# Kernel tuning notes

Hardware: AMD Instinct MI355X
Metric: run time of the kernel (lower is better)

Reference implementation:

```python
import jax, jax.numpy as jnp
import numpy as np

D_MODEL = 768
NHEAD = 12
HEAD_DIM = D_MODEL // NHEAD


def setup_inputs() -> dict:
    key = jax.random.key(0)
    ks = jax.random.split(key, 9)
    B, T = 4, 2048
    s = 1.0 / np.sqrt(D_MODEL)
    inp = {
        "x": jax.random.normal(ks[0], (B, T, D_MODEL), dtype=jnp.float32),
        "Wq": jax.random.normal(ks[1], (D_MODEL, D_MODEL), dtype=jnp.float32) * s,
        "bq": jnp.zeros((D_MODEL,), dtype=jnp.float32),
        "Wk": jax.random.normal(ks[2], (D_MODEL, D_MODEL), dtype=jnp.float32) * s,
        "bk": jnp.zeros((D_MODEL,), dtype=jnp.float32),
        "Wv": jax.random.normal(ks[3], (D_MODEL, D_MODEL), dtype=jnp.float32) * s,
        "bv": jnp.zeros((D_MODEL,), dtype=jnp.float32),
        "Wo": jax.random.normal(ks[4], (D_MODEL, D_MODEL), dtype=jnp.float32) * s,
        "bo": jnpp_zeros(ks) if False else jnp.zeros((D_MODEL,), dtype=jnp.float32),
    }
    return inp


def reference(x, Wq, bq, Wk, bk, Wv, bv, Wo, bo):
    B, T, _ = x.shape
    # projections (torch Linear: y = x @ W.T + b; here W stored as [in, out])
    q = (x @ Wq + bq).reshape(B, T, NHEAD, HEAD_DIM).transpose(0, 2, 1, 3)
    k = (x @ Wk + bk).reshape(B, T, NHEAD, HEAD_DIM).transpose(0, 2, 1, 3)
    v = (x @ Wv + bv).reshape(B, T, NHEAD, HEAD_DIM).transpose(0, 2, 1, 3)
    scale = 1.0 / np.sqrt(HEAD_DIM).astype(np.float32)
    scores = jnp.einsum("bhqd,bhkd->bhqk", q, k) * scale  # [B,H,T,T]
    attn = jax.nn.softmax(scores, axis=-1)
    out = jnp.einsum("bhqk,bhkd->bhqd", attn, v)  # [B,H,T,hd]
    out = out.transpose(0, 2, 1, 3).reshape(B, T, D_MODEL)
    return out @ Wo + bo
```

## Files before the change

### kernel.cpp

```cpp
#include <hip/hip_runtime.h>
#include <hip/hip_bf16.h>

#define DM 768
#define HD 64
#define NH 12
#define TT 2048
#define BB 4
#define MM 8192
#define BHH 48

typedef short bfx8 __attribute__((ext_vector_type(8)));
typedef short bfx4 __attribute__((ext_vector_type(4)));
typedef float f32x4 __attribute__((ext_vector_type(4)));
typedef float f32x16 __attribute__((ext_vector_type(16)));
typedef int i32x4 __attribute__((ext_vector_type(4)));
typedef unsigned uix2 __attribute__((ext_vector_type(2)));

__device__ __forceinline__ unsigned short f2bf(float f) {
  unsigned u = __float_as_uint(f);
  u += 0x7fffu + ((u >> 16) & 1u);
  return (unsigned short)(u >> 16);
}

__device__ __forceinline__ unsigned short f2bf_hw(float f) {
  return __builtin_bit_cast(unsigned short, __float2bfloat16(f));
}

__device__ __forceinline__ float fexp2(float x) {
#if __has_builtin(__builtin_amdgcn_exp2f)
  return __builtin_amdgcn_exp2f(x);
#else
  return __expf(x * 0.6931471805599453f);
#endif
}

__device__ __forceinline__ unsigned cvt_pk_bf16(float lo, float hi) {
  unsigned r;
  asm("v_cvt_pk_bf16_f32 %0, %1, %2" : "=v"(r) : "v"(lo), "v"(hi));
  return r;
}

__device__ __forceinline__ void pl32swap(unsigned& a, unsigned& b) {
#if __has_builtin(__builtin_amdgcn_permlane32_swap)
  uix2 r = __builtin_amdgcn_permlane32_swap(a, b, false, false);
  a = r.x; b = r.y;
#else
  asm volatile("v_permlane32_swap_b32 %0, %1" : "+v"(a), "+v"(b));
#endif
}

typedef const __attribute__((address_space(1))) void* gas_p;
typedef __attribute__((address_space(3))) void* las_p;
__device__ __forceinline__ void gld16(const void* g, void* l) {
  __builtin_amdgcn_global_load_lds((gas_p)g, (las_p)l, 16, 0, 0);
}

__global__ __launch_bounds__(256) void xconv(const float* __restrict__ x,
                                             short* __restrict__ xb, int n4) {
  int i = blockIdx.x * blockDim.x + threadIdx.x;
  int stride = gridDim.x * blockDim.x;
  for (; i < n4; i += stride) {
    float4 v = ((const float4*)x)[i];
    short4 o;
    o.x = (short)f2bf(v.x); o.y = (short)f2bf(v.y);
    o.z = (short)f2bf(v.z); o.w = (short)f2bf(v.w);
    ((short4*)xb)[i] = o;
  }
}

__global__ __launch_bounds__(256) void wconv_all(
    const float* __restrict__ W0, const float* __restrict__ W1,
    const float* __restrict__ W2, const float* __restrict__ W3,
    short* __restrict__ WtBase) {
  __shared__ float tile[32][33];
  int z = blockIdx.z;
  const float* W = z == 0 ? W0 : z == 1 ? W1 : z == 2 ? W2 : W3;
  short* Wt = WtBase + (size_t)z * (DM * DM);
  int kb = blockIdx.x * 32, nb = blockIdx.y * 32;
  int tx = threadIdx.x, ty = threadIdx.y;
#pragma unroll
  for (int i = 0; i < 4; ++i)
    tile[ty + 8 * i][tx] = W[(kb + ty + 8 * i) * DM + nb + tx];
  __syncthreads();
#pragma unroll
  for (int i = 0; i < 4; ++i)
    Wt[(nb + ty + 8 * i) * DM + kb + tx] = (short)f2bf(tile[tx][ty + 8 * i]);
}

template <int QKV>
__global__ __launch_bounds__(256) void gemm_k(
    const short* __restrict__ A, const short* __restrict__ Bt0,
    const float* __restrict__ b0, const float* __restrict__ b1,
    const float* __restrict__ b2, void* __restrict__ o0,
    void* __restrict__ o1, void* __restrict__ o2) {
  __shared__ __align__(16) short As[2][128 * 32];
  __shared__ __align__(16) short Bs[2][128 * 32];
  const int tid = threadIdx.x;
  const int lane = tid & 63, w = tid >> 6;
  const int ln15 = lane & 15, lg = lane >> 4;
  const int ny = blockIdx.y;
  const int mat = QKV ? (ny / 6) : 0;
  const int n0 = QKV ? (ny % 6) * 128 : ny * 128;
  const int mode = QKV ? (mat == 2 ? 1 : 0) : 2;
  const short* Bt = Bt0 + (size_t)mat * (DM * DM);
  const float* bias = QKV ? (mat == 0 ? b0 : mat == 1 ? b1 : b2) : b0;
  void* out = QKV ? (mat == 0 ? o0 : mat == 1 ? o1 : o2) : o0;
  const int m0 = blockIdx.x * 128;
  const int wm = w >> 1, wn = w & 1;

  f32x4 acc[4][4];
#pragma unroll
  for (int i = 0; i < 4; ++i)
#pragma unroll
    for (int j = 0; j < 4; ++j) acc[i][j] = f32x4{0.f, 0.f, 0.f, 0.f};

  auto stage = [&](int buf, int k0) {
#pragma unroll
    for (int j = 0; j < 2; ++j) {
      int c = w * 128 + j * 64 + lane;
      int row = c >> 2, cb = c & 3;
      int scb = cb ^ ((row >> 1) & 3);
      gld16(A + (m0 + row) * DM + k0 + (scb << 3), &As[buf][(w * 128 + j * 64) * 8]);
      gld16(Bt + (n0 + row) * DM + k0 + (scb << 3), &Bs[buf][(w * 128 + j * 64) * 8]);
    }
  };

  stage(0, 0);
  __syncthreads();

  for (int t = 0; t < 24; ++t) {
    int buf = t & 1;
    if (t + 1 < 24) stage(buf ^ 1, (t + 1) * 32);
    bfx8 af[4], bfr[4];
#pragma unroll
    for (int mt = 0; mt < 4; ++mt) {
      int row = wm * 64 + mt * 16 + ln15;
      int byt = (lg * 16) ^ (((row >> 1) & 3) << 4);
      af[mt] = *(const bfx8*)(&As[buf][row * 32 + (byt >> 1)]);
    }
#pragma unroll
    for (int nt = 0; nt < 4; ++nt) {
      int row = wn * 64 + nt * 16 + ln15;
      int byt = (lg * 16) ^ (((row >> 1) & 3) << 4);
      bfr[nt] = *(const bfx8*)(&Bs[buf][row * 32 + (byt >> 1)]);
    }
#pragma unroll
    for (int mt = 0; mt < 4; ++mt)
#pragma unroll
      for (int nt = 0; nt < 4; ++nt)
        acc[mt][nt] = __builtin_amdgcn_mfma_f32_16x16x32_bf16(af[mt], bfr[nt], acc[mt][nt], 0, 0, 0);
    __syncthreads();
  }

  float bv[4];
#pragma unroll
  for (int nt = 0; nt < 4; ++nt) bv[nt] = bias[n0 + wn * 64 + nt * 16 + ln15];

#pragma unroll
  for (int mt = 0; mt < 4; ++mt) {
#pragma unroll
    for (int nt = 0; nt < 4; ++nt) {
      int n = n0 + wn * 64 + nt * 16 + ln15;
      int mbase = m0 + wm * 64 + mt * 16 + lg * 4;
      if (mode == 2) {
        float* fo = (float*)out;
#pragma unroll
        for (int r = 0; r < 4; ++r)
          fo[(long)(mbase + r) * DM + n] = acc[mt][nt][r] + bv[nt];
      } else {
        short* so = (short*)out;
        int b = mbase >> 11, tt = mbase & 2047, h = n >> 6, d = n & 63;
        if (mode == 0) {
#pragma unroll
          for (int r = 0; r < 4; ++r)
            so[((long)(b * NH + h) * TT + tt + r) * HD + d] = (short)f2bf(acc[mt][nt][r] + bv[nt]);
        } else {
          bfx4 pk;
#pragma unroll
          for (int r = 0; r < 4; ++r) pk[r] = (short)f2bf(acc[mt][nt][r] + bv[nt]);
          *(bfx4*)(&so[((long)(b * NH + h) * HD + d) * TT + tt]) = pk;
        }
      }
    }
  }
}

__global__ __launch_bounds__(256) void attn_fwd(
    const short* __restrict__ Q, const short* __restrict__ K,
    const short* __restrict__ Vt, short* __restrict__ O) {
  __shared__ __align__(16) short Ks[2][64 * 64];
  __shared__ __align__(16) short Vs[2][64 * 64];
  const int tid = threadIdx.x, lane = tid & 63, w = tid >> 6;
  const int l31 = lane & 31, hi = lane >> 5;
  const int qt = blockIdx.x, bh = blockIdx.y;
  const int q0 = qt * 128 + w * 32;
  const short* Kh = K + (long)bh * TT * HD;
  const short* Vh = Vt + (long)bh * HD * TT;
  const float CEXP = 0.18033688011112042f;
  const float BIAS = 8.0f;

  bfx8 qf[4];
#pragma unroll
  for (int c = 0; c < 4; ++c)
    qf[c] = *(const bfx8*)(Q + ((long)bh * TT + q0 + l31) * HD + c * 16 + hi * 8);

  const int sw = (l31 & 7) << 4;
  const int base0 = l31 * 128, base1 = base0 + 4096;
  int col[4];
#pragma unroll
  for (int c = 0; c < 4; ++c) col[c] = (c * 32 + hi * 16) ^ sw;

  const short* kg[2];
  const short* vg[2];
#pragma unroll
  for (int j = 0; j < 2; ++j) {
    int c = w * 128 + j * 64 + lane;
    int row = c >> 3, cb = c & 7, scb = cb ^ (row & 7);
    kg[j] = Kh + row * HD + scb * 8;
    vg[j] = Vh + (long)row * TT + scb * 8;
  }

  auto stage = [&](int buf) {
#pragma unroll
    for (int j = 0; j < 2; ++j) {
      gld16(kg[j], (char*)Ks + buf * 8192 + (w * 128 + j * 64) * 16);
      gld16(vg[j], (char*)Vs + buf * 8192 + (w * 128 + j * 64) * 16);
    }
    kg[0] += 64 * HD; kg[1] += 64 * HD;
    vg[0] += 64;      vg[1] += 64;
  };

  f32x16 oacc[2];
#pragma unroll
  for (int db = 0; db < 2; ++db)
#pragma unroll
    for (int i = 0; i < 16; ++i) oacc[db][i] = 0.f;
  float lp = 0.f;

  stage(0);
  __syncthreads();

#pragma unroll 1
  for (int tp = 0; tp < 16; ++tp) {
#pragma unroll
    for (int half = 0; half < 2; ++half) {
      const int t = tp * 2 + half;
      if (t + 1 < 32) stage(half ^ 1);
      const char* ksb = (const char*)Ks + half * 8192;
      const char* vsb = (const char*)Vs + half * 8192;

      f32x16 sacc[2];
#pragma unroll
      for (int kvb = 0; kvb < 2; ++kvb) {
        f32x16 s;
#pragma unroll
        for (int i = 0; i < 16; ++i) s[i] = 0.f;
        const int rb = kvb ? base1 : base0;
#pragma unroll
        for (int c = 0; c < 4; ++c) {
          bfx8 kf = *(const bfx8*)(ksb + rb + col[c]);
          s = __builtin_amdgcn_mfma_f32_32x32x16_bf16(kf, qf[c], s, 0, 0, 0);
        }
        sacc[kvb] = s;
      }

      bfx8 pf[4];
#pragma unroll
      for (int kvb = 0; kvb < 2; ++kvb) {
        float pv[16];
#pragma unroll
        for (int r = 0; r < 16; ++r) {
          pv[r] = fexp2(__builtin_fmaf(sacc[kvb][r], CEXP, -BIAS));
          lp += pv[r];
        }
        unsigned g0a = cvt_pk_bf16(pv[0], pv[1]),   g0b = cvt_pk_bf16(pv[2], pv[3]);
        unsigned g1a = cvt_pk_bf16(pv[4], pv[5]),   g1b = cvt_pk_bf16(pv[6], pv[7]);
        unsigned g2a = cvt_pk_bf16(pv[8], pv[9]),   g2b = cvt_pk_bf16(pv[10], pv[11]);
        unsigned g3a = cvt_pk_bf16(pv[12], pv[13]), g3b = cvt_pk_bf16(pv[14], pv[15]);
        pl32swap(g0a, g1a); pl32swap(g0b, g1b);
        pl32swap(g2a, g3a); pl32swap(g2b, g3b);
        i32x4 f0 = {(int)g0a, (int)g0b, (int)g1a, (int)g1b};
        i32x4 f1 = {(int)g2a, (int)g2b, (int)g3a, (int)g3b};
        pf[kvb * 2]     = __builtin_bit_cast(bfx8, f0);
        pf[kvb * 2 + 1] = __builtin_bit_cast(bfx8, f1);
      }

#pragma unroll
      for (int db = 0; db < 2; ++db) {
        const int rb = db ? base1 : base0;
#pragma unroll
        for (int kt = 0; kt < 4; ++kt) {
          bfx8 vf = *(const bfx8*)(vsb + rb + col[kt]);
          oacc[db] = __builtin_amdgcn_mfma_f32_32x32x16_bf16(pf[kt], vf, oacc[db], 0, 0, 0);
        }
      }
      __syncthreads();
    }
  }

  lp += __shfl_xor(lp, 32);
  float linv = 1.f / lp;
  float lv[16];
#pragma unroll
  for (int g = 0; g < 4; ++g)
#pragma unroll
    for (int r = 0; r < 4; ++r) lv[g * 4 + r] = __shfl(linv, 8 * g + 4 * hi + r);
  const int b = bh / NH, h = bh - b * NH;
#pragma unroll
  for (int db = 0; db < 2; ++db)
#pragma unroll
    for (int g = 0; g < 4; ++g)
#pragma unroll
      for (int r = 0; r < 4; ++r) {
        int q = q0 + 8 * g + 4 * hi + r;
        O[(long)(b * TT + q) * DM + h * HD + db * 32 + l31] =
            (short)f2bf_hw(oacc[db][g * 4 + r] * lv[g * 4 + r]);
      }
}

extern "C" void kernel_launch(void* const* d_in, const int* in_sizes, int n_in,
                              void* d_out, int out_size, void* d_ws, size_t ws_size,
                              hipStream_t stream) {
  const float* x  = (const float*)d_in[0];
  const float* Wq = (const float*)d_in[1];
  const float* bq = (const float*)d_in[2];
  const float* Wk = (const float*)d_in[3];
  const float* bk = (const float*)d_in[4];
  const float* Wv = (const float*)d_in[5];
  const float* bv = (const float*)d_in[6];
  const float* Wo = (const float*)d_in[7];
  const float* bo = (const float*)d_in[8];
  float* out = (float*)d_out;

  char* ws = (char*)d_ws;
  short* xb  = (short*)(ws);
  short* WqT = (short*)(ws + 12582912);
  short* WoT = (short*)(ws + 16121856);
  short* Qb  = (short*)(ws + 17301504);
  short* Kb  = (short*)(ws + 29884416);
  short* Vtb = (short*)(ws + 42467328);
  short* Ob  = xb;

  xconv<<<2048, 256, 0, stream>>>(x, xb, MM * DM / 4);
  wconv_all<<<dim3(24, 24, 4), dim3(32, 8), 0, stream>>>(Wq, Wk, Wv, Wo, WqT);
  gemm_k<1><<<dim3(64, 18), 256, 0, stream>>>(xb, WqT, bq, bk, bv, Qb, Kb, Vtb);
  attn_fwd<<<dim3(16, BHH), 256, 0, stream>>>(Qb, Kb, Vtb, Ob);
  gemm_k<0><<<dim3(64, 6), 256, 0, stream>>>(Ob, WoT, bo, bo, bo, out, out, out);
}
```

Measured before the change: 236.5 us.

## Restructure attention to 64 queries per wave, read V from global, fuse prep kernels

The attention kernel now runs two waves per block, and each wave handles 64 queries (two 32-row tiles). Every K fragment loaded from LDS therefore feeds two MFMAs. V is no longer staged in LDS: it is read straight from global memory into registers, which halves LDS use per block. The block index is remapped so blocks that share a head are grouped together for L2 locality. The x and weight conversion kernels are merged into one launch to save a kernel launch. In exchange, register pressure rises and V loads are now exposed to global latency.

```diff
diff --git a/kernel.cpp b/kernel.cpp
--- a/kernel.cpp
+++ b/kernel.cpp
@@ -55,36 +55,41 @@
   __builtin_amdgcn_global_load_lds((gas_p)g, (las_p)l, 16, 0, 0);
 }
 
-__global__ __launch_bounds__(256) void xconv(const float* __restrict__ x,
-                                             short* __restrict__ xb, int n4) {
-  int i = blockIdx.x * blockDim.x + threadIdx.x;
-  int stride = gridDim.x * blockDim.x;
-  for (; i < n4; i += stride) {
-    float4 v = ((const float4*)x)[i];
-    short4 o;
-    o.x = (short)f2bf(v.x); o.y = (short)f2bf(v.y);
-    o.z = (short)f2bf(v.z); o.w = (short)f2bf(v.w);
-    ((short4*)xb)[i] = o;
-  }
-}
-
-__global__ __launch_bounds__(256) void wconv_all(
+__global__ __launch_bounds__(256) void prep(
+    const float* __restrict__ x, short* __restrict__ xb,
     const float* __restrict__ W0, const float* __restrict__ W1,
     const float* __restrict__ W2, const float* __restrict__ W3,
     short* __restrict__ WtBase) {
-  __shared__ float tile[32][33];
-  int z = blockIdx.z;
-  const float* W = z == 0 ? W0 : z == 1 ? W1 : z == 2 ? W2 : W3;
-  short* Wt = WtBase + (size_t)z * (DM * DM);
-  int kb = blockIdx.x * 32, nb = blockIdx.y * 32;
-  int tx = threadIdx.x, ty = threadIdx.y;
-#pragma unroll
-  for (int i = 0; i < 4; ++i)
-    tile[ty + 8 * i][tx] = W[(kb + ty + 8 * i) * DM + nb + tx];
-  __syncthreads();
-#pragma unroll
-  for (int i = 0; i < 4; ++i)
-    Wt[(nb + ty + 8 * i) * DM + kb + tx] = (short)f2bf(tile[tx][ty + 8 * i]);
+  const int bid = blockIdx.x, tid = threadIdx.x;
+  if (bid < 2304) {
+    __shared__ float tile[32][33];
+    int z = bid / 576, rem = bid % 576;
+    const float* W = z == 0 ? W0 : z == 1 ? W1 : z == 2 ? W2 : W3;
+    short* Wt = WtBase + (size_t)z * (DM * DM);
+    int kb = (rem % 24) * 32, nb = (rem / 24) * 32;
+    int tx = tid & 31, ty = tid >> 5;
+#pragma unroll
+    for (int i = 0; i < 4; ++i)
+      tile[ty + 8 * i][tx] = W[(kb + ty + 8 * i) * DM + nb + tx];
+    __syncthreads();
+#pragma unroll
+    for (int i = 0; i < 4; ++i)
+      Wt[(nb + ty + 8 * i) * DM + kb + tx] = (short)f2bf(tile[tx][ty + 8 * i]);
+  } else {
+    const int n4 = MM * DM / 4;
+    int i = (bid - 2304) * 256 + tid;
+    const int stride = 1536 * 256;
+#pragma unroll
+    for (int it = 0; it < 4; ++it, i += stride) {
+      if (i < n4) {
+        float4 v = ((const float4*)x)[i];
+        short4 o;
+        o.x = (short)f2bf(v.x); o.y = (short)f2bf(v.y);
+        o.z = (short)f2bf(v.z); o.w = (short)f2bf(v.w);
+        ((short4*)xb)[i] = o;
+      }
+    }
+  }
 }
 
 template <int QKV>
@@ -185,24 +190,28 @@
   }
 }
 
-__global__ __launch_bounds__(256) void attn_fwd(
+__global__ __launch_bounds__(128, 2) void attn_fwd(
     const short* __restrict__ Q, const short* __restrict__ K,
     const short* __restrict__ Vt, short* __restrict__ O) {
   __shared__ __align__(16) short Ks[2][64 * 64];
-  __shared__ __align__(16) short Vs[2][64 * 64];
   const int tid = threadIdx.x, lane = tid & 63, w = tid >> 6;
   const int l31 = lane & 31, hi = lane >> 5;
-  const int qt = blockIdx.x, bh = blockIdx.y;
-  const int q0 = qt * 128 + w * 32;
+  const int id = blockIdx.x;
+  const int s = id >> 3;
+  const int bh = (id & 7) * 6 + (s % 6);
+  const int qt = s / 6;
+  const int q0 = qt * 128 + w * 64;
   const short* Kh = K + (long)bh * TT * HD;
   const short* Vh = Vt + (long)bh * HD * TT;
   const float CEXP = 0.18033688011112042f;
   const float BIAS = 8.0f;
 
-  bfx8 qf[4];
-#pragma unroll
-  for (int c = 0; c < 4; ++c)
-    qf[c] = *(const bfx8*)(Q + ((long)bh * TT + q0 + l31) * HD + c * 16 + hi * 8);
+  bfx8 qf[2][4];
+#pragma unroll
+  for (int qb = 0; qb < 2; ++qb)
+#pragma unroll
+    for (int c = 0; c < 4; ++c)
+      qf[qb][c] = *(const bfx8*)(Q + ((long)bh * TT + q0 + qb * 32 + l31) * HD + c * 16 + hi * 8);
 
   const int sw = (l31 & 7) << 4;
   const int base0 = l31 * 128, base1 = base0 + 4096;
@@ -210,32 +219,32 @@
 #pragma unroll
   for (int c = 0; c < 4; ++c) col[c] = (c * 32 + hi * 16) ^ sw;
 
-  const short* kg[2];
-  const short* vg[2];
-#pragma unroll
-  for (int j = 0; j < 2; ++j) {
-    int c = w * 128 + j * 64 + lane;
-    int row = c >> 3, cb = c & 7, scb = cb ^ (row & 7);
-    kg[j] = Kh + row * HD + scb * 8;
-    vg[j] = Vh + (long)row * TT + scb * 8;
-  }
-
+  const short* kg[4];
+#pragma unroll
+  for (int p = 0; p < 4; ++p) {
+    int chunk = p * 128 + tid;
+    int row = chunk >> 3, slot = chunk & 7, sslot = slot ^ (row & 7);
+    kg[p] = Kh + row * HD + sslot * 8;
+  }
   auto stage = [&](int buf) {
 #pragma unroll
-    for (int j = 0; j < 2; ++j) {
-      gld16(kg[j], (char*)Ks + buf * 8192 + (w * 128 + j * 64) * 16);
-      gld16(vg[j], (char*)Vs + buf * 8192 + (w * 128 + j * 64) * 16);
-    }
-    kg[0] += 64 * HD; kg[1] += 64 * HD;
-    vg[0] += 64;      vg[1] += 64;
+    for (int p = 0; p < 4; ++p) {
+      gld16(kg[p], (char*)Ks + buf * 8192 + (p * 128 + tid) * 16);
+      kg[p] += 64 * HD;
+    }
   };
 
-  f32x16 oacc[2];
-#pragma unroll
-  for (int db = 0; db < 2; ++db)
-#pragma unroll
-    for (int i = 0; i < 16; ++i) oacc[db][i] = 0.f;
-  float lp = 0.f;
+  const short* vp0 = Vh + (long)(l31) * TT + hi * 8;
+  const short* vp1 = Vh + (long)(32 + l31) * TT + hi * 8;
+
+  f32x16 oacc[2][2];
+#pragma unroll
+  for (int qb = 0; qb < 2; ++qb)
+#pragma unroll
+    for (int db = 0; db < 2; ++db)
+#pragma unroll
+      for (int i = 0; i < 16; ++i) oacc[qb][db][i] = 0.f;
+  float lp0 = 0.f, lp1 = 0.f;
 
   stage(0);
   __syncthreads();
@@ -247,75 +256,81 @@
       const int t = tp * 2 + half;
       if (t + 1 < 32) stage(half ^ 1);
       const char* ksb = (const char*)Ks + half * 8192;
-      const char* vsb = (const char*)Vs + half * 8192;
-
-      f32x16 sacc[2];
+
+      bfx8 vf[2][4];
+#pragma unroll
+      for (int ktg = 0; ktg < 4; ++ktg) {
+        vf[0][ktg] = *(const bfx8*)(vp0 + ktg * 16);
+        vf[1][ktg] = *(const bfx8*)(vp1 + ktg * 16);
+      }
+      vp0 += 64; vp1 += 64;
+
 #pragma unroll
       for (int kvb = 0; kvb < 2; ++kvb) {
-        f32x16 s;
-#pragma unroll
-        for (int i = 0; i < 16; ++i) s[i] = 0.f;
         const int rb = kvb ? base1 : base0;
+        f32x16 s0, s1;
+#pragma unroll
+        for (int i = 0; i < 16; ++i) { s0[i] = 0.f; s1[i] = 0.f; }
 #pragma unroll
         for (int c = 0; c < 4; ++c) {
           bfx8 kf = *(const bfx8*)(ksb + rb + col[c]);
-          s = __builtin_amdgcn_mfma_f32_32x32x16_bf16(kf, qf[c], s, 0, 0, 0);
+          s0 = __builtin_amdgcn_mfma_f32_32x32x16_bf16(kf, qf[0][c], s0, 0, 0, 0);
+          s1 = __builtin_amdgcn_mfma_f32_32x32x16_bf16(kf, qf[1][c], s1, 0, 0, 0);
         }
-        sacc[kvb] = s;
-      }
-
-      bfx8 pf[4];
-#pragma unroll
-      for (int kvb = 0; kvb < 2; ++kvb) {
-        float pv[16];
-#pragma unroll
-        for (int r = 0; r < 16; ++r) {
-          pv[r] = fexp2(__builtin_fmaf(sacc[kvb][r], CEXP, -BIAS));
-          lp += pv[r];
-        }
-        unsigned g0a = cvt_pk_bf16(pv[0], pv[1]),   g0b = cvt_pk_bf16(pv[2], pv[3]);
-        unsigned g1a = cvt_pk_bf16(pv[4], pv[5]),   g1b = cvt_pk_bf16(pv[6], pv[7]);
-        unsigned g2a = cvt_pk_bf16(pv[8], pv[9]),   g2b = cvt_pk_bf16(pv[10], pv[11]);
-        unsigned g3a = cvt_pk_bf16(pv[12], pv[13]), g3b = cvt_pk_bf16(pv[14], pv[15]);
-        pl32swap(g0a, g1a); pl32swap(g0b, g1b);
-        pl32swap(g2a, g3a); pl32swap(g2b, g3b);
-        i32x4 f0 = {(int)g0a, (int)g0b, (int)g1a, (int)g1b};
-        i32x4 f1 = {(int)g2a, (int)g2b, (int)g3a, (int)g3b};
-        pf[kvb * 2]     = __builtin_bit_cast(bfx8, f0);
-        pf[kvb * 2 + 1] = __builtin_bit_cast(bfx8, f1);
-      }
-
-#pragma unroll
-      for (int db = 0; db < 2; ++db) {
-        const int rb = db ? base1 : base0;
-#pragma unroll
-        for (int kt = 0; kt < 4; ++kt) {
-          bfx8 vf = *(const bfx8*)(vsb + rb + col[kt]);
-          oacc[db] = __builtin_amdgcn_mfma_f32_32x32x16_bf16(pf[kt], vf, oacc[db], 0, 0, 0);
+#pragma unroll
+        for (int qb = 0; qb < 2; ++qb) {
+          const f32x16& sv = qb ? s1 : s0;
+          float pv[16];
+          float rs = 0.f;
+#pragma unroll
+          for (int r = 0; r < 16; ++r) {
+            pv[r] = fexp2(__builtin_fmaf(sv[r], CEXP, -BIAS));
+            rs += pv[r];
+          }
+          if (qb) lp1 += rs; else lp0 += rs;
+          unsigned g0a = cvt_pk_bf16(pv[0], pv[1]),   g0b = cvt_pk_bf16(pv[2], pv[3]);
+          unsigned g1a = cvt_pk_bf16(pv[4], pv[5]),   g1b = cvt_pk_bf16(pv[6], pv[7]);
+          unsigned g2a = cvt_pk_bf16(pv[8], pv[9]),   g2b = cvt_pk_bf16(pv[10], pv[11]);
+          unsigned g3a = cvt_pk_bf16(pv[12], pv[13]), g3b = cvt_pk_bf16(pv[14], pv[15]);
+          pl32swap(g0a, g1a); pl32swap(g0b, g1b);
+          pl32swap(g2a, g3a); pl32swap(g2b, g3b);
+          i32x4 f0 = {(int)g0a, (int)g0b, (int)g1a, (int)g1b};
+          i32x4 f1 = {(int)g2a, (int)g2b, (int)g3a, (int)g3b};
+          bfx8 pfA = __builtin_bit_cast(bfx8, f0);
+          bfx8 pfB = __builtin_bit_cast(bfx8, f1);
+          const int k0i = kvb * 2, k1i = kvb * 2 + 1;
+          oacc[qb][0] = __builtin_amdgcn_mfma_f32_32x32x16_bf16(pfA, vf[0][k0i], oacc[qb][0], 0, 0, 0);
+          oacc[qb][0] = __builtin_amdgcn_mfma_f32_32x32x16_bf16(pfB, vf[0][k1i], oacc[qb][0], 0, 0, 0);
+          oacc[qb][1] = __builtin_amdgcn_mfma_f32_32x32x16_bf16(pfA, vf[1][k0i], oacc[qb][1], 0, 0, 0);
+          oacc[qb][1] = __builtin_amdgcn_mfma_f32_32x32x16_bf16(pfB, vf[1][k1i], oacc[qb][1], 0, 0, 0);
         }
       }
       __syncthreads();
     }
   }
 
-  lp += __shfl_xor(lp, 32);
-  float linv = 1.f / lp;
-  float lv[16];
-#pragma unroll
-  for (int g = 0; g < 4; ++g)
-#pragma unroll
-    for (int r = 0; r < 4; ++r) lv[g * 4 + r] = __shfl(linv, 8 * g + 4 * hi + r);
   const int b = bh / NH, h = bh - b * NH;
 #pragma unroll
-  for (int db = 0; db < 2; ++db)
+  for (int qb = 0; qb < 2; ++qb) {
+    float lp = qb ? lp1 : lp0;
+    lp += __shfl_xor(lp, 32);
+    float linv = 1.f / lp;
+    float lv[16];
 #pragma unroll
     for (int g = 0; g < 4; ++g)
 #pragma unroll
-      for (int r = 0; r < 4; ++r) {
-        int q = q0 + 8 * g + 4 * hi + r;
-        O[(long)(b * TT + q) * DM + h * HD + db * 32 + l31] =
-            (short)f2bf_hw(oacc[db][g * 4 + r] * lv[g * 4 + r]);
-      }
+      for (int r = 0; r < 4; ++r) lv[g * 4 + r] = __shfl(linv, 8 * g + 4 * hi + r);
+#pragma unroll
+    for (int db = 0; db < 2; ++db)
+#pragma unroll
+      for (int g = 0; g < 4; ++g)
+#pragma unroll
+        for (int r = 0; r < 4; ++r) {
+          int q = q0 + qb * 32 + 8 * g + 4 * hi + r;
+          O[(long)(b * TT + q) * DM + h * HD + db * 32 + l31] =
+              (short)f2bf_hw(oacc[qb][db][g * 4 + r] * lv[g * 4 + r]);
+        }
+  }
 }
 
 extern "C" void kernel_launch(void* const* d_in, const int* in_sizes, int n_in,
@@ -341,9 +356,8 @@
   short* Vtb = (short*)(ws + 42467328);
   short* Ob  = xb;
 
-  xconv<<<2048, 256, 0, stream>>>(x, xb, MM * DM / 4);
-  wconv_all<<<dim3(24, 24, 4), dim3(32, 8), 0, stream>>>(Wq, Wk, Wv, Wo, WqT);
+  prep<<<3840, 256, 0, stream>>>(x, xb, Wq, Wk, Wv, Wo, WqT);
   gemm_k<1><<<dim3(64, 18), 256, 0, stream>>>(xb, WqT, bq, bk, bv, Qb, Kb, Vtb);
-  attn_fwd<<<dim3(16, BHH), 256, 0, stream>>>(Qb, Kb, Vtb, Ob);
+  attn_fwd<<<768, 128, 0, stream>>>(Qb, Kb, Vtb, Ob);
   gemm_k<0><<<dim3(64, 6), 256, 0, stream>>>(Ob, WoT, bo, bo, bo, out, out, out);
 }
```

Result: no change. 235.1 us (-0.6%).
